# Kernel tuning notes

Measured on AMD Instinct MI355X. Metric: run time of the kernel, lower is better.

Reference implementation:

```python
import jax, jax.numpy as jnp
import numpy as np

B, S, DIM = 2, 2048, 1024
HID = 2048          # multiple_of-rounded hidden dim
E, NSH, TOPK = 8, 2, 2


def _ffn(x, w1, w2, w3):
    return (jax.nn.silu(x @ w1.T) * (x @ w3.T)) @ w2.T


def setup_inputs() -> dict:
    key = jax.random.key(0)
    ks = jax.random.split(key, 8)
    sc = 0.02  # init scale for stability
    return {
        "x": jax.random.normal(ks[0], (B, S, DIM), jnp.float32),
        "router_w": jax.random.normal(ks[1], (E, DIM), jnp.float32) * sc,
        "expert_bias": jnp.zeros((E,), jnp.float32),
        "w1": jax.random.normal(ks[2], (E, HID, DIM), jnp.float32) * sc,
        "w3": jax.random.normal(ks[3], (E, HID, DIM), jnp.float32) * sc,
        "w2": jax.random.normal(ks[4], (E, DIM, HID), jnp.float32) * sc,
        "sw1": jax.random.normal(ks[5], (NSH, HID, DIM), jnp.float32) * sc,
        "sw3": jax.random.normal(ks[6], (NSH, HID, DIM), jnp.float32) * sc,
        "sw2": jax.random.normal(ks[7], (NSH, DIM, HID), jnp.float32) * sc,
    }


def reference(x, router_w, expert_bias, w1, w3, w2, sw1, sw3, sw2):
    bs, sl, d = x.shape
    xf = x.reshape(-1, d)  # [T, d]

    # shared experts (always-on)
    shared = jnp.zeros_like(xf)
    for i in range(sw1.shape[0]):
        shared = shared + _ffn(xf, sw1[i], sw2[i], sw3[i])

    # router with aux-free load-balance bias
    logits = xf @ router_w.T + expert_bias  # [T, E]
    rw, sel = jax.lax.top_k(logits, TOPK)   # [T, K]
    rw = jax.nn.softmax(rw.astype(jnp.float32), axis=-1).astype(x.dtype)

    # combine weights per (token, expert): sum of routing weights over topk slots
    onehot = jax.nn.one_hot(sel, E, dtype=x.dtype)        # [T, K, E]
    combine = jnp.einsum('tk,tke->te', rw, onehot)        # [T, E]

    # per-expert FFN accumulated via scan (equivalent to gather-FFN-scatter)
    def body(acc, ew):
        e1, e3, e2, cw = ew  # cw: [T]
        acc = acc + cw[:, None] * _ffn(xf, e1, e2, e3)
        return acc, None

    out, _ = jax.lax.scan(body, jnp.zeros_like(xf), (w1, w3, w2, combine.T))
    out = out + shared
    return out.reshape(bs, sl, -1)
```

## Files before the change

kernel.cpp:

```cpp
#include <hip/hip_runtime.h>
#include <stdint.h>

#define T_TOK 4096
#define DIMD  1024
#define HIDN  2048
#define NEXP  8
#define RMAX  9216

typedef float f32x4 __attribute__((ext_vector_type(4)));
typedef short s16x8 __attribute__((ext_vector_type(8)));

__device__ __forceinline__ uint16_t f2bf(float f) {
    uint32_t u = __builtin_bit_cast(uint32_t, f);
    u += 0x7fffu + ((u >> 16) & 1u);
    return (uint16_t)(u >> 16);
}
__device__ __forceinline__ float bf2f(uint32_t h) {
    return __builtin_bit_cast(float, h << 16);
}
__device__ __forceinline__ uint32_t pk2(float a, float b) {
    return (uint32_t)f2bf(a) | ((uint32_t)f2bf(b) << 16);
}
__device__ __forceinline__ int swz(int r, int cbyte) {
    return r * 128 + (cbyte ^ ((r & 7) << 4));
}
__device__ __forceinline__ void gload16(const void* g, void* l) {
    __builtin_amdgcn_global_load_lds(
        (const __attribute__((address_space(1))) void*)g,
        (__attribute__((address_space(3))) void*)l, 16, 0, 0);
}
__device__ __forceinline__ void stage128x64(const uint16_t* gbase, int ldk,
                                            char* lds, int wv, int lane) {
    #pragma unroll
    for (int i = 0; i < 4; ++i) {
        int s = (wv * 4 + i) * 64 + lane;
        int row = s >> 3;
        int cb = ((s & 7) << 4) ^ ((row & 7) << 4);
        gload16(gbase + (size_t)row * ldk + (cb >> 1), lds + ((wv * 4 + i) << 10));
    }
}


struct CvtArgs {
    const float* s[7];
    uint16_t*    d[7];
    int          nq[7];
};

__global__ void cvt_all_kernel(CvtArgs a) {
    int base = blockIdx.x * blockDim.x + threadIdx.x;
    int stride = gridDim.x * blockDim.x;
    #pragma unroll
    for (int seg = 0; seg < 7; ++seg) {
        const float4* sp = (const float4*)a.s[seg];
        uint2* dp = (uint2*)a.d[seg];
        int n = a.nq[seg];
        for (int i = base; i < n; i += stride) {
            float4 v = sp[i];
            uint2 o; o.x = pk2(v.x, v.y); o.y = pk2(v.z, v.w);
            dp[i] = o;
        }
    }
}

__global__ __launch_bounds__(256)
void router_kernel(const float* __restrict__ x, const float* __restrict__ rw,
                   const float* __restrict__ bias,
                   int* __restrict__ sel, float* __restrict__ wgt,
                   int* __restrict__ cnt) {
    __shared__ float rws[NEXP * DIMD];
    int tid = threadIdx.x;
    for (int i = tid; i < NEXP * DIMD / 4; i += 256)
        ((float4*)rws)[i] = ((const float4*)rw)[i];
    __syncthreads();

    int wid = tid >> 6, lane = tid & 63;
    float b[NEXP];
    #pragma unroll
    for (int e = 0; e < NEXP; ++e) b[e] = bias[e];

    int t0 = (blockIdx.x * 4 + wid) * 8;
    for (int j = 0; j < 8; ++j) {
        int t = t0 + j;
        const float4* xr = (const float4*)(x + (size_t)t * DIMD);
        float p[NEXP] = {};
        #pragma unroll
        for (int c = 0; c < 4; ++c) {
            float4 xv = xr[c * 64 + lane];
            #pragma unroll
            for (int e = 0; e < NEXP; ++e) {
                float4 wv = *(const float4*)(rws + e * DIMD + c * 256 + lane * 4);
                p[e] += xv.x * wv.x + xv.y * wv.y + xv.z * wv.z + xv.w * wv.w;
            }
        }
        #pragma unroll
        for (int off = 32; off >= 1; off >>= 1) {
            #pragma unroll
            for (int e = 0; e < NEXP; ++e) p[e] += __shfl_xor(p[e], off, 64);
        }
        if (lane == 0) {
            #pragma unroll
            for (int e = 0; e < NEXP; ++e) p[e] += b[e];
            float l0 = -1e30f; int i0 = 0;
            #pragma unroll
            for (int e = 0; e < NEXP; ++e) { if (p[e] > l0) { l0 = p[e]; i0 = e; } }
            float l1 = -1e30f; int i1 = 0;
            #pragma unroll
            for (int e = 0; e < NEXP; ++e) { if (e == i0) continue; if (p[e] > l1) { l1 = p[e]; i1 = e; } }
            float e1 = expf(l1 - l0);
            float d = 1.f + e1;
            sel[t * 2] = i0; sel[t * 2 + 1] = i1;
            wgt[t * 2] = 1.f / d; wgt[t * 2 + 1] = e1 / d;
            atomicAdd(&cnt[i0], 1);
            atomicAdd(&cnt[i1], 1);
        }
    }
}

__global__ void offs_kernel(const int* __restrict__ cnt, int* __restrict__ offs) {
    if (threadIdx.x == 0 && blockIdx.x == 0) {
        int o = 0;
        for (int e = 0; e < NEXP; ++e) { offs[e] = o; o += (cnt[e] + 127) & ~127; }
        offs[NEXP] = o;
    }
}

__global__ void assign_kernel(const int* __restrict__ sel, const int* __restrict__ offs,
                              int* __restrict__ fill, int* __restrict__ row_of) {
    int i = blockIdx.x * blockDim.x + threadIdx.x;
    if (i < T_TOK * 2) {
        int e = sel[i];
        row_of[i] = offs[e] + atomicAdd(&fill[e], 1);
    }
}

__global__ void gather_kernel(const uint16_t* __restrict__ xb, const int* __restrict__ row_of,
                              uint16_t* __restrict__ Xg) {
    int slot = blockIdx.x;
    int pos = row_of[slot];
    int t = slot >> 1;
    const uint4* src = (const uint4*)(xb + (size_t)t * DIMD);
    uint4* dst = (uint4*)(Xg + (size_t)pos * DIMD);
    dst[threadIdx.x] = src[threadIdx.x];
}

__global__ void combine_kernel(const uint16_t* __restrict__ H2g, const int* __restrict__ row_of,
                               const float* __restrict__ wgt, float* __restrict__ out) {
    int t = blockIdx.x;
    int c = threadIdx.x * 8;
    int r0 = row_of[t * 2], r1 = row_of[t * 2 + 1];
    float w0 = wgt[t * 2], w1 = wgt[t * 2 + 1];
    uint4 a = *(const uint4*)(H2g + (size_t)r0 * DIMD + c);
    uint4 b = *(const uint4*)(H2g + (size_t)r1 * DIMD + c);
    float* o = out + (size_t)t * DIMD + c;
    o[0] += w0 * bf2f(a.x & 0xffffu) + w1 * bf2f(b.x & 0xffffu);
    o[1] += w0 * bf2f(a.x >> 16)     + w1 * bf2f(b.x >> 16);
    o[2] += w0 * bf2f(a.y & 0xffffu) + w1 * bf2f(b.y & 0xffffu);
    o[3] += w0 * bf2f(a.y >> 16)     + w1 * bf2f(b.y >> 16);
    o[4] += w0 * bf2f(a.z & 0xffffu) + w1 * bf2f(b.z & 0xffffu);
    o[5] += w0 * bf2f(a.z >> 16)     + w1 * bf2f(b.z >> 16);
    o[6] += w0 * bf2f(a.w & 0xffffu) + w1 * bf2f(b.w & 0xffffu);
    o[7] += w0 * bf2f(a.w >> 16)     + w1 * bf2f(b.w >> 16);
}


template<int ROUTED>
__global__ __launch_bounds__(256, 2)
void gemm13_kernel(const uint16_t* __restrict__ A,
                   const uint16_t* __restrict__ W1, const uint16_t* __restrict__ W3,
                   uint16_t* __restrict__ H, int ldh,
                   const int* __restrict__ offs) {
    __shared__ __align__(16) char lds[49152];
    char* As  = lds;
    char* B1s = lds + 16384;
    char* B3s = lds + 32768;

    const int K = DIMD;
    int row0 = blockIdx.y * 128;
    const uint16_t *b1 = W1, *b3 = W3;
    if (ROUTED) {
        if (row0 >= offs[NEXP]) return;
        int e = 0;
        while (row0 >= offs[e + 1]) ++e;
        size_t eo = (size_t)e * HIDN * DIMD;
        b1 += eo; b3 += eo;
    }
    int col0 = blockIdx.x * 128;

    int tid = threadIdx.x, lane = tid & 63;
    int wv = tid >> 6, wm = wv >> 1, wn = wv & 1;

    f32x4 acc1[4][4] = {};
    f32x4 acc3[4][4] = {};

    for (int kt = 0; kt < K; kt += 64) {
        __syncthreads();
        stage128x64(A  + (size_t)row0 * K + kt, K, As,  wv, lane);
        stage128x64(b1 + (size_t)col0 * K + kt, K, B1s, wv, lane);
        stage128x64(b3 + (size_t)col0 * K + kt, K, B3s, wv, lane);
        __syncthreads();

        #pragma unroll
        for (int s = 0; s < 2; ++s) {
            int cb = s * 64 + ((lane >> 4) << 4);
            s16x8 av[4];
            #pragma unroll
            for (int i = 0; i < 4; ++i)
                av[i] = *(const s16x8*)(As + swz(wm * 64 + i * 16 + (lane & 15), cb));
            #pragma unroll
            for (int j = 0; j < 4; ++j) {
                int br = wn * 64 + j * 16 + (lane & 15);
                s16x8 bv1 = *(const s16x8*)(B1s + swz(br, cb));
                s16x8 bv3 = *(const s16x8*)(B3s + swz(br, cb));
                #pragma unroll
                for (int i = 0; i < 4; ++i) {
                    acc1[i][j] = __builtin_amdgcn_mfma_f32_16x16x32_bf16(av[i], bv1, acc1[i][j], 0, 0, 0);
                    acc3[i][j] = __builtin_amdgcn_mfma_f32_16x16x32_bf16(av[i], bv3, acc3[i][j], 0, 0, 0);
                }
            }
        }
    }

    #pragma unroll
    for (int i = 0; i < 4; ++i) {
        #pragma unroll
        for (int j = 0; j < 4; ++j) {
            #pragma unroll
            for (int rg = 0; rg < 4; ++rg) {
                int row = row0 + wm * 64 + i * 16 + ((lane >> 4) << 2) + rg;
                int col = col0 + wn * 64 + j * 16 + (lane & 15);
                float a1 = acc1[i][j][rg];
                float a3 = acc3[i][j][rg];
                float hv = (a1 / (1.f + __expf(-a1))) * a3;
                H[(size_t)row * ldh + col] = f2bf(hv);
            }
        }
    }
}

template<int ROUTED>
__global__ __launch_bounds__(256, 3)
void gemm2_kernel(const uint16_t* __restrict__ A, int lda,
                  const uint16_t* __restrict__ W2, void* __restrict__ Cout,
                  const int* __restrict__ offs,
                  int K, int kSplit, long long expStride) {
    __shared__ __align__(16) char lds[32768];
    char* As = lds;
    char* Bs = lds + 16384;

    int row0 = blockIdx.y * 128;
    const uint16_t* b2 = W2;
    if (ROUTED) {
        if (row0 >= offs[NEXP]) return;
        int e = 0;
        while (row0 >= offs[e + 1]) ++e;
        b2 += (size_t)e * DIMD * HIDN;
    }
    int col0 = blockIdx.x * 128;

    int tid = threadIdx.x, lane = tid & 63;
    int wv = tid >> 6, wm = wv >> 1, wn = wv & 1;

    f32x4 acc[4][4] = {};

    for (int kt = 0; kt < K; kt += 64) {
        const uint16_t* bb = b2 + (size_t)(kt / kSplit) * expStride + (kt % kSplit);
        __syncthreads();
        stage128x64(A  + (size_t)row0 * lda + kt, lda, As, wv, lane);
        stage128x64(bb + (size_t)col0 * kSplit, kSplit, Bs, wv, lane);
        __syncthreads();

        #pragma unroll
        for (int s = 0; s < 2; ++s) {
            int cb = s * 64 + ((lane >> 4) << 4);
            s16x8 av[4];
            #pragma unroll
            for (int i = 0; i < 4; ++i)
                av[i] = *(const s16x8*)(As + swz(wm * 64 + i * 16 + (lane & 15), cb));
            #pragma unroll
            for (int j = 0; j < 4; ++j) {
                s16x8 bv = *(const s16x8*)(Bs + swz(wn * 64 + j * 16 + (lane & 15), cb));
                #pragma unroll
                for (int i = 0; i < 4; ++i)
                    acc[i][j] = __builtin_amdgcn_mfma_f32_16x16x32_bf16(av[i], bv, acc[i][j], 0, 0, 0);
            }
        }
    }

    #pragma unroll
    for (int i = 0; i < 4; ++i) {
        #pragma unroll
        for (int j = 0; j < 4; ++j) {
            #pragma unroll
            for (int rg = 0; rg < 4; ++rg) {
                int row = row0 + wm * 64 + i * 16 + ((lane >> 4) << 2) + rg;
                int col = col0 + wn * 64 + j * 16 + (lane & 15);
                float v = acc[i][j][rg];
                if (ROUTED) ((uint16_t*)Cout)[(size_t)row * DIMD + col] = f2bf(v);
                else        ((float*)Cout)[(size_t)row * DIMD + col] += v;
            }
        }
    }
}


extern "C" void kernel_launch(void* const* d_in, const int* in_sizes, int n_in,
                              void* d_out, int out_size, void* d_ws, size_t ws_size,
                              hipStream_t stream) {
    const float* x   = (const float*)d_in[0];
    const float* rw  = (const float*)d_in[1];
    const float* eb  = (const float*)d_in[2];
    const float* w1  = (const float*)d_in[3];
    const float* w3  = (const float*)d_in[4];
    const float* w2  = (const float*)d_in[5];
    const float* sw1 = (const float*)d_in[6];
    const float* sw3 = (const float*)d_in[7];
    const float* sw2 = (const float*)d_in[8];
    float* out = (float*)d_out;

    const int EW = NEXP * HIDN * DIMD;
    const int SW = 2 * HIDN * DIMD;

    char* ws = (char*)d_ws;
    size_t off = 0;
    auto alloc = [&](size_t b) { char* p = ws + off; off = (off + b + 255) & ~(size_t)255; return p; };
    uint16_t* xb  = (uint16_t*)alloc((size_t)T_TOK * DIMD * 2);
    uint16_t* Xg  = (uint16_t*)alloc((size_t)RMAX * DIMD * 2);
    uint16_t* Hg  = (uint16_t*)alloc((size_t)RMAX * HIDN * 2);
    uint16_t* H2g = (uint16_t*)alloc((size_t)RMAX * DIMD * 2);
    uint16_t* w1b = (uint16_t*)alloc((size_t)EW * 2);
    uint16_t* w3b = (uint16_t*)alloc((size_t)EW * 2);
    uint16_t* w2b = (uint16_t*)alloc((size_t)EW * 2);
    uint16_t* sw1b = (uint16_t*)alloc((size_t)SW * 2);
    uint16_t* sw3b = (uint16_t*)alloc((size_t)SW * 2);
    uint16_t* sw2b = (uint16_t*)alloc((size_t)SW * 2);
    int*   sel    = (int*)  alloc(T_TOK * 2 * 4);
    float* wgt    = (float*)alloc(T_TOK * 2 * 4);
    int*   row_of = (int*)  alloc(T_TOK * 2 * 4);
    int*   cnt    = (int*)  alloc(64);
    int*   fill   = (int*)  alloc(64);
    int*   offs   = (int*)  alloc(64);

    hipMemsetAsync(cnt, 0, 64, stream);
    hipMemsetAsync(fill, 0, 64, stream);
    hipMemsetAsync(Xg, 0, (size_t)RMAX * DIMD * 2, stream);
    hipMemsetAsync(out, 0, (size_t)out_size * sizeof(float), stream);

    CvtArgs ca;
    ca.s[0] = w1;  ca.d[0] = w1b;  ca.nq[0] = EW / 4;
    ca.s[1] = w3;  ca.d[1] = w3b;  ca.nq[1] = EW / 4;
    ca.s[2] = w2;  ca.d[2] = w2b;  ca.nq[2] = EW / 4;
    ca.s[3] = sw1; ca.d[3] = sw1b; ca.nq[3] = SW / 4;
    ca.s[4] = sw3; ca.d[4] = sw3b; ca.nq[4] = SW / 4;
    ca.s[5] = sw2; ca.d[5] = sw2b; ca.nq[5] = SW / 4;
    ca.s[6] = x;   ca.d[6] = xb;   ca.nq[6] = T_TOK * DIMD / 4;
    cvt_all_kernel<<<2048, 256, 0, stream>>>(ca);

    router_kernel<<<128, 256, 0, stream>>>(x, rw, eb, sel, wgt, cnt);
    offs_kernel<<<1, 1, 0, stream>>>(cnt, offs);
    assign_kernel<<<32, 256, 0, stream>>>(sel, offs, fill, row_of);
    gather_kernel<<<T_TOK * 2, 128, 0, stream>>>(xb, row_of, Xg);

    gemm13_kernel<1><<<dim3(HIDN / 128, RMAX / 128), 256, 0, stream>>>(Xg, w1b, w3b, Hg, HIDN, offs);
    gemm2_kernel<1><<<dim3(DIMD / 128, RMAX / 128), 256, 0, stream>>>(Hg, HIDN, w2b, (void*)H2g, offs,
                                                                      HIDN, HIDN, 0);
    combine_kernel<<<T_TOK, 128, 0, stream>>>(H2g, row_of, wgt, out);

    gemm13_kernel<0><<<dim3((2 * HIDN) / 128, T_TOK / 128), 256, 0, stream>>>(xb, sw1b, sw3b, Hg, 2 * HIDN, nullptr);
    gemm2_kernel<0><<<dim3(DIMD / 128, T_TOK / 128), 256, 0, stream>>>(Hg, 2 * HIDN, sw2b, (void*)out, nullptr,
                                                                       2 * HIDN, HIDN, (long long)DIMD * HIDN);
}
```

Measured before the change: 557.0 us.

## Merge shared experts into routed grouped GEMM with gather-on-load and single combine

Shared experts are treated as two extra experts appended after the routed rows, so one gemm13 launch and one gemm2 launch cover routed and shared work together. The separate gather kernel and the Xg buffer are dropped; the A-tile load now reads token rows directly through a tok index. The combine kernel sums the routed and shared outputs and writes the result once, which removes the memset of out and the fp32 read-modify-write. In exchange the shared path now goes through bf16 H2 before summation, adding rounding error, and the first kernel reads A rows through an indirection.

```diff
diff --git a/kernel.cpp b/kernel.cpp
--- a/kernel.cpp
+++ b/kernel.cpp
@@ -6,6 +6,7 @@
 #define HIDN  2048
 #define NEXP  8
 #define RMAX  9216
+#define RROWS (RMAX + 2 * T_TOK)
 
 typedef float f32x4 __attribute__((ext_vector_type(4)));
 typedef short s16x8 __attribute__((ext_vector_type(8)));
@@ -126,50 +127,51 @@
 }
 
 __global__ void assign_kernel(const int* __restrict__ sel, const int* __restrict__ offs,
-                              int* __restrict__ fill, int* __restrict__ row_of) {
+                              int* __restrict__ fill, int* __restrict__ row_of,
+                              int* __restrict__ tok) {
     int i = blockIdx.x * blockDim.x + threadIdx.x;
-    if (i < T_TOK * 2) {
+    if (i < 2 * T_TOK) {
         int e = sel[i];
-        row_of[i] = offs[e] + atomicAdd(&fill[e], 1);
-    }
-}
-
-__global__ void gather_kernel(const uint16_t* __restrict__ xb, const int* __restrict__ row_of,
-                              uint16_t* __restrict__ Xg) {
-    int slot = blockIdx.x;
-    int pos = row_of[slot];
-    int t = slot >> 1;
-    const uint4* src = (const uint4*)(xb + (size_t)t * DIMD);
-    uint4* dst = (uint4*)(Xg + (size_t)pos * DIMD);
-    dst[threadIdx.x] = src[threadIdx.x];
-}
-
-__global__ void combine_kernel(const uint16_t* __restrict__ H2g, const int* __restrict__ row_of,
-                               const float* __restrict__ wgt, float* __restrict__ out) {
+        int r = offs[e] + atomicAdd(&fill[e], 1);
+        row_of[i] = r;
+        tok[r] = i >> 1;
+    } else if (i < 4 * T_TOK) {
+        int j = i - 2 * T_TOK;
+        tok[offs[NEXP] + j] = j & (T_TOK - 1);
+    }
+}
+
+__global__ void combine_kernel(const uint16_t* __restrict__ H2, const int* __restrict__ row_of,
+                               const float* __restrict__ wgt, const int* __restrict__ offs,
+                               float* __restrict__ out) {
     int t = blockIdx.x;
     int c = threadIdx.x * 8;
     int r0 = row_of[t * 2], r1 = row_of[t * 2 + 1];
+    int s0 = offs[NEXP] + t, s1 = s0 + T_TOK;
     float w0 = wgt[t * 2], w1 = wgt[t * 2 + 1];
-    uint4 a = *(const uint4*)(H2g + (size_t)r0 * DIMD + c);
-    uint4 b = *(const uint4*)(H2g + (size_t)r1 * DIMD + c);
+    uint4 a = *(const uint4*)(H2 + (size_t)r0 * DIMD + c);
+    uint4 b = *(const uint4*)(H2 + (size_t)r1 * DIMD + c);
+    uint4 u = *(const uint4*)(H2 + (size_t)s0 * DIMD + c);
+    uint4 v = *(const uint4*)(H2 + (size_t)s1 * DIMD + c);
+    float4 o0, o1;
+    o0.x = w0 * bf2f(a.x & 0xffffu) + w1 * bf2f(b.x & 0xffffu) + bf2f(u.x & 0xffffu) + bf2f(v.x & 0xffffu);
+    o0.y = w0 * bf2f(a.x >> 16)     + w1 * bf2f(b.x >> 16)     + bf2f(u.x >> 16)     + bf2f(v.x >> 16);
+    o0.z = w0 * bf2f(a.y & 0xffffu) + w1 * bf2f(b.y & 0xffffu) + bf2f(u.y & 0xffffu) + bf2f(v.y & 0xffffu);
+    o0.w = w0 * bf2f(a.y >> 16)     + w1 * bf2f(b.y >> 16)     + bf2f(u.y >> 16)     + bf2f(v.y >> 16);
+    o1.x = w0 * bf2f(a.z & 0xffffu) + w1 * bf2f(b.z & 0xffffu) + bf2f(u.z & 0xffffu) + bf2f(v.z & 0xffffu);
+    o1.y = w0 * bf2f(a.z >> 16)     + w1 * bf2f(b.z >> 16)     + bf2f(u.z >> 16)     + bf2f(v.z >> 16);
+    o1.z = w0 * bf2f(a.w & 0xffffu) + w1 * bf2f(b.w & 0xffffu) + bf2f(u.w & 0xffffu) + bf2f(v.w & 0xffffu);
+    o1.w = w0 * bf2f(a.w >> 16)     + w1 * bf2f(b.w >> 16)     + bf2f(u.w >> 16)     + bf2f(v.w >> 16);
     float* o = out + (size_t)t * DIMD + c;
-    o[0] += w0 * bf2f(a.x & 0xffffu) + w1 * bf2f(b.x & 0xffffu);
-    o[1] += w0 * bf2f(a.x >> 16)     + w1 * bf2f(b.x >> 16);
-    o[2] += w0 * bf2f(a.y & 0xffffu) + w1 * bf2f(b.y & 0xffffu);
-    o[3] += w0 * bf2f(a.y >> 16)     + w1 * bf2f(b.y >> 16);
-    o[4] += w0 * bf2f(a.z & 0xffffu) + w1 * bf2f(b.z & 0xffffu);
-    o[5] += w0 * bf2f(a.z >> 16)     + w1 * bf2f(b.z >> 16);
-    o[6] += w0 * bf2f(a.w & 0xffffu) + w1 * bf2f(b.w & 0xffffu);
-    o[7] += w0 * bf2f(a.w >> 16)     + w1 * bf2f(b.w >> 16);
-}
-
-
-template<int ROUTED>
+    *(float4*)o = o0;
+    *(float4*)(o + 4) = o1;
+}
+
+
 __global__ __launch_bounds__(256, 2)
-void gemm13_kernel(const uint16_t* __restrict__ A,
+void gemm13_kernel(const uint16_t* __restrict__ xb, const int* __restrict__ tok,
                    const uint16_t* __restrict__ W1, const uint16_t* __restrict__ W3,
-                   uint16_t* __restrict__ H, int ldh,
-                   const int* __restrict__ offs) {
+                   uint16_t* __restrict__ H, const int* __restrict__ offs) {
     __shared__ __align__(16) char lds[49152];
     char* As  = lds;
     char* B1s = lds + 16384;
@@ -177,25 +179,39 @@
 
     const int K = DIMD;
     int row0 = blockIdx.y * 128;
-    const uint16_t *b1 = W1, *b3 = W3;
-    if (ROUTED) {
-        if (row0 >= offs[NEXP]) return;
-        int e = 0;
+    int rsh = row0 - offs[NEXP];
+    int e;
+    if (rsh >= 0) {
+        if (rsh >= 2 * T_TOK) return;
+        e = NEXP + (rsh >> 12);
+    } else {
+        e = 0;
         while (row0 >= offs[e + 1]) ++e;
-        size_t eo = (size_t)e * HIDN * DIMD;
-        b1 += eo; b3 += eo;
-    }
+    }
+    const uint16_t* b1 = W1 + (size_t)e * HIDN * DIMD;
+    const uint16_t* b3 = W3 + (size_t)e * HIDN * DIMD;
     int col0 = blockIdx.x * 128;
 
     int tid = threadIdx.x, lane = tid & 63;
     int wv = tid >> 6, wm = wv >> 1, wn = wv & 1;
 
+    size_t abase[4];
+    #pragma unroll
+    for (int i = 0; i < 4; ++i) {
+        int s = (wv * 4 + i) * 64 + lane;
+        int row = s >> 3;
+        int cb = ((s & 7) << 4) ^ ((row & 7) << 4);
+        abase[i] = (size_t)tok[row0 + row] * DIMD + (cb >> 1);
+    }
+
     f32x4 acc1[4][4] = {};
     f32x4 acc3[4][4] = {};
 
     for (int kt = 0; kt < K; kt += 64) {
         __syncthreads();
-        stage128x64(A  + (size_t)row0 * K + kt, K, As,  wv, lane);
+        #pragma unroll
+        for (int i = 0; i < 4; ++i)
+            gload16(xb + abase[i] + kt, As + ((wv * 4 + i) << 10));
         stage128x64(b1 + (size_t)col0 * K + kt, K, B1s, wv, lane);
         stage128x64(b3 + (size_t)col0 * K + kt, K, B3s, wv, lane);
         __syncthreads();
@@ -232,30 +248,32 @@
                 float a1 = acc1[i][j][rg];
                 float a3 = acc3[i][j][rg];
                 float hv = (a1 / (1.f + __expf(-a1))) * a3;
-                H[(size_t)row * ldh + col] = f2bf(hv);
-            }
-        }
-    }
-}
-
-template<int ROUTED>
+                H[(size_t)row * HIDN + col] = f2bf(hv);
+            }
+        }
+    }
+}
+
 __global__ __launch_bounds__(256, 3)
-void gemm2_kernel(const uint16_t* __restrict__ A, int lda,
-                  const uint16_t* __restrict__ W2, void* __restrict__ Cout,
-                  const int* __restrict__ offs,
-                  int K, int kSplit, long long expStride) {
+void gemm2_kernel(const uint16_t* __restrict__ Hg,
+                  const uint16_t* __restrict__ W2, uint16_t* __restrict__ H2,
+                  const int* __restrict__ offs) {
     __shared__ __align__(16) char lds[32768];
     char* As = lds;
     char* Bs = lds + 16384;
 
+    const int K = HIDN;
     int row0 = blockIdx.y * 128;
-    const uint16_t* b2 = W2;
-    if (ROUTED) {
-        if (row0 >= offs[NEXP]) return;
-        int e = 0;
+    int rsh = row0 - offs[NEXP];
+    int e;
+    if (rsh >= 0) {
+        if (rsh >= 2 * T_TOK) return;
+        e = NEXP + (rsh >> 12);
+    } else {
+        e = 0;
         while (row0 >= offs[e + 1]) ++e;
-        b2 += (size_t)e * DIMD * HIDN;
-    }
+    }
+    const uint16_t* b2 = W2 + (size_t)e * DIMD * HIDN;
     int col0 = blockIdx.x * 128;
 
     int tid = threadIdx.x, lane = tid & 63;
@@ -264,10 +282,9 @@
     f32x4 acc[4][4] = {};
 
     for (int kt = 0; kt < K; kt += 64) {
-        const uint16_t* bb = b2 + (size_t)(kt / kSplit) * expStride + (kt % kSplit);
         __syncthreads();
-        stage128x64(A  + (size_t)row0 * lda + kt, lda, As, wv, lane);
-        stage128x64(bb + (size_t)col0 * kSplit, kSplit, Bs, wv, lane);
+        stage128x64(Hg + (size_t)row0 * K + kt, K, As, wv, lane);
+        stage128x64(b2 + (size_t)col0 * K + kt, K, Bs, wv, lane);
         __syncthreads();
 
         #pragma unroll
@@ -295,9 +312,7 @@
             for (int rg = 0; rg < 4; ++rg) {
                 int row = row0 + wm * 64 + i * 16 + ((lane >> 4) << 2) + rg;
                 int col = col0 + wn * 64 + j * 16 + (lane & 15);
-                float v = acc[i][j][rg];
-                if (ROUTED) ((uint16_t*)Cout)[(size_t)row * DIMD + col] = f2bf(v);
-                else        ((float*)Cout)[(size_t)row * DIMD + col] += v;
+                H2[(size_t)row * DIMD + col] = f2bf(acc[i][j][rg]);
             }
         }
     }
@@ -324,49 +339,40 @@
     char* ws = (char*)d_ws;
     size_t off = 0;
     auto alloc = [&](size_t b) { char* p = ws + off; off = (off + b + 255) & ~(size_t)255; return p; };
-    uint16_t* xb  = (uint16_t*)alloc((size_t)T_TOK * DIMD * 2);
-    uint16_t* Xg  = (uint16_t*)alloc((size_t)RMAX * DIMD * 2);
-    uint16_t* Hg  = (uint16_t*)alloc((size_t)RMAX * HIDN * 2);
-    uint16_t* H2g = (uint16_t*)alloc((size_t)RMAX * DIMD * 2);
-    uint16_t* w1b = (uint16_t*)alloc((size_t)EW * 2);
-    uint16_t* w3b = (uint16_t*)alloc((size_t)EW * 2);
-    uint16_t* w2b = (uint16_t*)alloc((size_t)EW * 2);
-    uint16_t* sw1b = (uint16_t*)alloc((size_t)SW * 2);
-    uint16_t* sw3b = (uint16_t*)alloc((size_t)SW * 2);
-    uint16_t* sw2b = (uint16_t*)alloc((size_t)SW * 2);
+    uint16_t* xb    = (uint16_t*)alloc((size_t)T_TOK * DIMD * 2);
+    uint16_t* Hg    = (uint16_t*)alloc((size_t)RROWS * HIDN * 2);
+    uint16_t* H2    = (uint16_t*)alloc((size_t)RROWS * DIMD * 2);
+    uint16_t* w1all = (uint16_t*)alloc((size_t)(EW + SW) * 2);
+    uint16_t* w3all = (uint16_t*)alloc((size_t)(EW + SW) * 2);
+    uint16_t* w2all = (uint16_t*)alloc((size_t)(EW + SW) * 2);
     int*   sel    = (int*)  alloc(T_TOK * 2 * 4);
     float* wgt    = (float*)alloc(T_TOK * 2 * 4);
     int*   row_of = (int*)  alloc(T_TOK * 2 * 4);
+    int*   tok    = (int*)  alloc(RROWS * 4);
     int*   cnt    = (int*)  alloc(64);
     int*   fill   = (int*)  alloc(64);
     int*   offs   = (int*)  alloc(64);
 
     hipMemsetAsync(cnt, 0, 64, stream);
     hipMemsetAsync(fill, 0, 64, stream);
-    hipMemsetAsync(Xg, 0, (size_t)RMAX * DIMD * 2, stream);
-    hipMemsetAsync(out, 0, (size_t)out_size * sizeof(float), stream);
+    hipMemsetAsync(tok, 0, RROWS * 4, stream);
 
     CvtArgs ca;
-    ca.s[0] = w1;  ca.d[0] = w1b;  ca.nq[0] = EW / 4;
-    ca.s[1] = w3;  ca.d[1] = w3b;  ca.nq[1] = EW / 4;
-    ca.s[2] = w2;  ca.d[2] = w2b;  ca.nq[2] = EW / 4;
-    ca.s[3] = sw1; ca.d[3] = sw1b; ca.nq[3] = SW / 4;
-    ca.s[4] = sw3; ca.d[4] = sw3b; ca.nq[4] = SW / 4;
-    ca.s[5] = sw2; ca.d[5] = sw2b; ca.nq[5] = SW / 4;
-    ca.s[6] = x;   ca.d[6] = xb;   ca.nq[6] = T_TOK * DIMD / 4;
+    ca.s[0] = w1;  ca.d[0] = w1all;      ca.nq[0] = EW / 4;
+    ca.s[1] = sw1; ca.d[1] = w1all + EW; ca.nq[1] = SW / 4;
+    ca.s[2] = w3;  ca.d[2] = w3all;      ca.nq[2] = EW / 4;
+    ca.s[3] = sw3; ca.d[3] = w3all + EW; ca.nq[3] = SW / 4;
+    ca.s[4] = w2;  ca.d[4] = w2all;      ca.nq[4] = EW / 4;
+    ca.s[5] = sw2; ca.d[5] = w2all + EW; ca.nq[5] = SW / 4;
+    ca.s[6] = x;   ca.d[6] = xb;         ca.nq[6] = T_TOK * DIMD / 4;
     cvt_all_kernel<<<2048, 256, 0, stream>>>(ca);
 
     router_kernel<<<128, 256, 0, stream>>>(x, rw, eb, sel, wgt, cnt);
     offs_kernel<<<1, 1, 0, stream>>>(cnt, offs);
-    assign_kernel<<<32, 256, 0, stream>>>(sel, offs, fill, row_of);
-    gather_kernel<<<T_TOK * 2, 128, 0, stream>>>(xb, row_of, Xg);
-
-    gemm13_kernel<1><<<dim3(HIDN / 128, RMAX / 128), 256, 0, stream>>>(Xg, w1b, w3b, Hg, HIDN, offs);
-    gemm2_kernel<1><<<dim3(DIMD / 128, RMAX / 128), 256, 0, stream>>>(Hg, HIDN, w2b, (void*)H2g, offs,
-                                                                      HIDN, HIDN, 0);
-    combine_kernel<<<T_TOK, 128, 0, stream>>>(H2g, row_of, wgt, out);
-
-    gemm13_kernel<0><<<dim3((2 * HIDN) / 128, T_TOK / 128), 256, 0, stream>>>(xb, sw1b, sw3b, Hg, 2 * HIDN, nullptr);
-    gemm2_kernel<0><<<dim3(DIMD / 128, T_TOK / 128), 256, 0, stream>>>(Hg, 2 * HIDN, sw2b, (void*)out, nullptr,
-                                                                       2 * HIDN, HIDN, (long long)DIMD * HIDN);
-}
+    assign_kernel<<<64, 256, 0, stream>>>(sel, offs, fill, row_of, tok);
+
+    gemm13_kernel<<<dim3(HIDN / 128, RROWS / 128), 256, 0, stream>>>(xb, tok, w1all, w3all, Hg, offs);
+    gemm2_kernel<<<dim3(DIMD / 128, RROWS / 128), 256, 0, stream>>>(Hg, w2all, H2, offs);
+
+    combine_kernel<<<T_TOK, 128, 0, stream>>>(H2, row_of, wgt, offs, out);
+}
```

Result: faster. 473.5 us (-15.0%).
